# Performance work log

Hardware: AMD Instinct MI355X
Metric: run time of the kernel (lower is better)

Reference implementation:

```python
import jax, jax.numpy as jnp
import numpy as np

B, N, F_IN, F_OUT, H = 8, 1024, 256, 256, 4
HD = F_OUT // H  # head_dim = 64
NEG_SLOPE = 0.2


def setup_inputs() -> dict:
    key = jax.random.key(0)
    k1, k2, k3 = jax.random.split(key, 3)
    x = jax.random.normal(k1, (B, N, F_IN), dtype=jnp.float32)
    adj = jnp.ones((B, N, N), dtype=jnp.int32)
    # Linear weight, stored as [in, out] so h = x @ W
    W = jax.random.normal(k2, (F_IN, F_OUT), dtype=jnp.float32) / np.sqrt(F_IN)
    # attention vector a: [H, 2*head_dim], xavier-ish init
    a = jax.random.normal(k3, (H, 2 * HD), dtype=jnp.float32) * np.sqrt(2.0 / (H + 2 * HD))
    return {"x": x, "adj": adj, "W": W, "a": a}


def reference(x, adj, W, a):
    Bq, Nq, _ = x.shape
    h = (x @ W).reshape(Bq, Nq, H, HD).transpose(0, 2, 1, 3)  # [B,H,N,HD]
    a1, a2 = a[:, :HD], a[:, HD:]  # decompose concat: e_nm = h_n.a1 + h_m.a2
    s1 = jnp.einsum('bhnd,hd->bhn', h, a1)
    s2 = jnp.einsum('bhmd,hd->bhm', h, a2)
    e = jax.nn.leaky_relu(s1[:, :, :, None] + s2[:, :, None, :], NEG_SLOPE)  # [B,H,N,N]
    e = jnp.where(adj[:, None, :, :] == 0, -jnp.inf, e)
    attention = jax.nn.softmax(e, axis=-1)
    out = jnp.einsum('bhnm,bhmd->bhnd', attention, h)
    return out.transpose(0, 2, 1, 3).reshape(Bq, Nq, H * HD)
```

## Files before the change

### kernel.cpp

```cpp
#include <hip/hip_runtime.h>
#include <math.h>

#define H 4
#define HD 64
#define NN 1024
#define BB 8
#define FIN 256
#define FOUT 256

typedef _Float16 f16x8 __attribute__((ext_vector_type(8)));
typedef _Float16 f16x4 __attribute__((ext_vector_type(4)));
typedef _Float16 f16x2 __attribute__((ext_vector_type(2)));
typedef float f32x4 __attribute__((ext_vector_type(4)));

__device__ __forceinline__ unsigned fkey(float f) {
  unsigned u = __float_as_uint(f);
  return (u & 0x80000000u) ? ~u : (u | 0x80000000u);
}
__device__ __forceinline__ float fdecode(unsigned k) {
  unsigned u = (k & 0x80000000u) ? (k & 0x7fffffffu) : ~k;
  return __uint_as_float(u);
}

__global__ __launch_bounds__(256) void prep(const int* __restrict__ adj,
                                            unsigned* __restrict__ adjP,
                                            const float* __restrict__ W,
                                            _Float16* __restrict__ WT,
                                            unsigned* __restrict__ S2maxU) {
  __shared__ float tile[64][68];
  const int tid = threadIdx.x;
  if (blockIdx.x < 1024) {
    size_t widx = (size_t)blockIdx.x * 256 + tid;
    const int4* p = (const int4*)adj + widx * 8;
    int4 v[8];
#pragma unroll
    for (int i = 0; i < 8; ++i) v[i] = p[i];
    unsigned bits = 0;
#pragma unroll
    for (int i = 0; i < 8; ++i) {
      bits |= (v[i].x != 0 ? 1u : 0u) << (4 * i);
      bits |= (v[i].y != 0 ? 2u : 0u) << (4 * i);
      bits |= (v[i].z != 0 ? 4u : 0u) << (4 * i);
      bits |= (v[i].w != 0 ? 8u : 0u) << (4 * i);
    }
    adjP[widx] = bits;
  } else {
    if (blockIdx.x == 1024 && tid < 32) S2maxU[tid] = 0u;
    const int bx = blockIdx.x - 1024;
    const int k0 = (bx & 3) * 64, f0 = (bx >> 2) * 64;
    const int r = tid >> 4, c4 = (tid & 15) * 4;
#pragma unroll
    for (int p = 0; p < 4; ++p) {
      float4 v = *(const float4*)&W[(size_t)(k0 + p * 16 + r) * FOUT + f0 + c4];
      *(float4*)&tile[p * 16 + r][c4] = v;
    }
    __syncthreads();
    const int f = tid >> 2, kg = (tid & 3) * 16;
#pragma unroll
    for (int i = 0; i < 4; ++i) {
      f16x4 o;
#pragma unroll
      for (int j = 0; j < 4; ++j) o[j] = (_Float16)tile[kg + i * 4 + j][f];
      *(f16x4*)&WT[(size_t)(f0 + f) * FIN + k0 + kg + i * 4] = o;
    }
  }
}

__global__ __launch_bounds__(256) void gemm_xw(const float* __restrict__ x,
                                               const _Float16* __restrict__ WT,
                                               const float* __restrict__ a,
                                               _Float16* __restrict__ hT,
                                               float* __restrict__ s1_ws,
                                               float* __restrict__ s2_ws,
                                               unsigned* __restrict__ S2maxU) {
  __shared__ _Float16 wl[64][264];
  const int tid = threadIdx.x;
  const int lane = tid & 63, w = tid >> 6;
  const int c = lane & 15, q = lane >> 4;
  const int bn0 = blockIdx.x * 64;
  const int head = blockIdx.y;
  const int b = bn0 >> 10, nb = bn0 & 1023;
  const int bh = b * H + head;

  {
    const int row = tid >> 2, kseg = (tid & 3) * 64;
    const _Float16* wp = WT + (size_t)(head * 64 + row) * FIN + kseg;
#pragma unroll
    for (int i = 0; i < 8; ++i) {
      f16x8 t = *(const f16x8*)(wp + i * 8);
      *(f16x8*)&wl[row][kseg + i * 8] = t;
    }
  }
  __syncthreads();

  f32x4 acc[4];
#pragma unroll
  for (int t = 0; t < 4; ++t) acc[t] = (f32x4){0.f, 0.f, 0.f, 0.f};
  const float* xp = x + (size_t)(bn0 + w * 16 + c) * FIN + q * 8;
#pragma unroll
  for (int ks = 0; ks < 8; ++ks) {
    float4 xa = *(const float4*)(xp + ks * 32);
    float4 xb = *(const float4*)(xp + ks * 32 + 4);
    f16x8 af;
    af[0] = (_Float16)xa.x; af[1] = (_Float16)xa.y;
    af[2] = (_Float16)xa.z; af[3] = (_Float16)xa.w;
    af[4] = (_Float16)xb.x; af[5] = (_Float16)xb.y;
    af[6] = (_Float16)xb.z; af[7] = (_Float16)xb.w;
#pragma unroll
    for (int t = 0; t < 4; ++t) {
      f16x8 bf = *(const f16x8*)&wl[t * 16 + c][ks * 32 + q * 8];
      acc[t] = __builtin_amdgcn_mfma_f32_16x16x32_f16(af, bf, acc[t], 0, 0, 0);
    }
  }

  float a1v[4], a2v[4];
#pragma unroll
  for (int t = 0; t < 4; ++t) {
    a1v[t] = a[head * 2 * HD + t * 16 + c];
    a2v[t] = a[head * 2 * HD + HD + t * 16 + c];
  }
  float s1p[4] = {0.f, 0.f, 0.f, 0.f};
  float s2p[4] = {0.f, 0.f, 0.f, 0.f};
#pragma unroll
  for (int t = 0; t < 4; ++t) {
    f16x4 hv;
#pragma unroll
    for (int rr = 0; rr < 4; ++rr) {
      hv[rr] = (_Float16)acc[t][rr];
      s1p[rr] += acc[t][rr] * a1v[t];
      s2p[rr] += acc[t][rr] * a2v[t];
    }
    *(f16x4*)&hT[((size_t)(bh * 64 + t * 16 + c)) * NN + nb + w * 16 + q * 4] = hv;
  }
  float ms2 = -INFINITY;
#pragma unroll
  for (int rr = 0; rr < 4; ++rr) {
    float s1 = s1p[rr], s2 = s2p[rr];
#pragma unroll
    for (int off = 8; off; off >>= 1) {
      s1 += __shfl_xor(s1, off);
      s2 += __shfl_xor(s2, off);
    }
    ms2 = fmaxf(ms2, s2);
    if (c == 0) {
      int n = nb + w * 16 + q * 4 + rr;
      size_t idx = (size_t)bh * NN + n;
      s1_ws[idx] = s1;
      s2_ws[idx] = s2;
    }
  }
  ms2 = fmaxf(ms2, __shfl_xor(ms2, 16));
  ms2 = fmaxf(ms2, __shfl_xor(ms2, 32));
  if (lane == 0) atomicMax(&S2maxU[bh], fkey(ms2));
}

__global__ __launch_bounds__(256) void attn(const _Float16* __restrict__ hT,
                                            const float* __restrict__ s1_ws,
                                            const float* __restrict__ s2_ws,
                                            const unsigned* __restrict__ S2maxU,
                                            const unsigned* __restrict__ adjP,
                                            float* __restrict__ out) {
  __shared__ _Float16 u16[NN], v16[NN];
  __shared__ unsigned adjW[64][36];
  __shared__ int denseFlag;
  const int tid = threadIdx.x, lane = tid & 63, wv = tid >> 6;
  const int c = lane & 15, q = lane >> 4;
  const int ntile = blockIdx.x, bh = blockIdx.y;
  const int b = bh >> 2, head = bh & 3;
  const int n0 = ntile * 64;

  if (tid == 0) denseFlag = 1;
  __syncthreads();

  const float S2 = fdecode(S2maxU[bh]);
  {
    float4 s2a = *(const float4*)&s2_ws[(size_t)bh * NN + tid * 4];
    f16x4 ua, va;
    ua[0] = (_Float16)__expf(s2a.x - S2); va[0] = (_Float16)__expf(0.2f * (s2a.x - S2));
    ua[1] = (_Float16)__expf(s2a.y - S2); va[1] = (_Float16)__expf(0.2f * (s2a.y - S2));
    ua[2] = (_Float16)__expf(s2a.z - S2); va[2] = (_Float16)__expf(0.2f * (s2a.z - S2));
    ua[3] = (_Float16)__expf(s2a.w - S2); va[3] = (_Float16)__expf(0.2f * (s2a.w - S2));
    *(f16x4*)&u16[tid * 4] = ua;
    *(f16x4*)&v16[tid * 4] = va;
    const int row = tid >> 2, wo = (tid & 3) * 8;
    const uint4* ap = (const uint4*)(adjP + ((size_t)(b * NN + n0 + row)) * 32 + wo);
    uint4 m0 = ap[0], m1 = ap[1];
    *(uint4*)&adjW[row][wo] = m0;
    *(uint4*)&adjW[row][wo + 4] = m1;
    unsigned andall = m0.x & m0.y & m0.z & m0.w & m1.x & m1.y & m1.z & m1.w;
    if (andall != 0xffffffffu) atomicAnd(&denseFlag, 0);
  }
  __syncthreads();
  const int dense = denseFlag;

  f16x2 ar2[4], br2[4];
#pragma unroll
  for (int g = 0; g < 4; ++g) {
    float s1 = s1_ws[(size_t)bh * NN + n0 + g * 16 + c];
    float t = s1 + S2;
    float M = fmaxf(t, 0.2f * t);
    _Float16 A = (_Float16)__expf(t - M);
    _Float16 Bv = (_Float16)__expf(0.2f * t - M);
    ar2[g][0] = A; ar2[g][1] = A;
    br2[g][0] = Bv; br2[g][1] = Bv;
  }

  f32x4 acc[4], accL[4];
#pragma unroll
  for (int g = 0; g < 4; ++g) {
    acc[g] = (f32x4){0.f, 0.f, 0.f, 0.f};
    accL[g] = (f32x4){0.f, 0.f, 0.f, 0.f};
  }
  f16x8 bones;
  {
    _Float16 o = (c == 0) ? (_Float16)1.0f : (_Float16)0.0f;
#pragma unroll
    for (int j = 0; j < 8; ++j) bones[j] = o;
  }

  const _Float16* bp = hT + ((size_t)bh * 64 + wv * 16 + c) * NN + q * 8;
  f16x8 nbf = *(const f16x8*)bp;

  for (int kc4 = 0; kc4 < 8; ++kc4) {
    unsigned mrow[4][4];
    if (!dense) {
#pragma unroll
      for (int g = 0; g < 4; ++g) {
        uint4 t = *(const uint4*)&adjW[g * 16 + c][kc4 * 4];
        mrow[g][0] = t.x; mrow[g][1] = t.y; mrow[g][2] = t.z; mrow[g][3] = t.w;
      }
    }
#pragma unroll
    for (int kk = 0; kk < 4; ++kk) {
      const int kc = kc4 * 4 + kk;
      f16x8 bf = nbf;
      if (kc < 31) nbf = *(const f16x8*)(bp + (kc + 1) * 32);
      f16x8 u8 = *(const f16x8*)&u16[kc * 32 + q * 8];
      f16x8 v8 = *(const f16x8*)&v16[kc * 32 + q * 8];
      f16x2 up[4], vp[4];
#pragma unroll
      for (int j = 0; j < 4; ++j) {
        up[j][0] = u8[2 * j]; up[j][1] = u8[2 * j + 1];
        vp[j][0] = v8[2 * j]; vp[j][1] = v8[2 * j + 1];
      }
#pragma unroll
      for (int g = 0; g < 4; ++g) {
        f16x2 pp[4];
#pragma unroll
        for (int j = 0; j < 4; ++j)
          pp[j] = __builtin_elementwise_max(ar2[g] * up[j], br2[g] * vp[j]);
        if (!dense) {
          unsigned byte = (mrow[g][kk] >> (q * 8)) & 0xffu;
#pragma unroll
          for (int j = 0; j < 4; ++j) {
            unsigned pm = __builtin_bit_cast(unsigned, pp[j]);
            unsigned msk = (((byte >> (2 * j)) & 1u) ? 0x0000ffffu : 0u) |
                           (((byte >> (2 * j + 1)) & 1u) ? 0xffff0000u : 0u);
            pp[j] = __builtin_bit_cast(f16x2, pm & msk);
          }
        }
        union { f16x8 v8_; f16x2 v2_[4]; } au;
        au.v2_[0] = pp[0]; au.v2_[1] = pp[1]; au.v2_[2] = pp[2]; au.v2_[3] = pp[3];
        acc[g] = __builtin_amdgcn_mfma_f32_16x16x32_f16(au.v8_, bf, acc[g], 0, 0, 0);
        accL[g] = __builtin_amdgcn_mfma_f32_16x16x32_f16(au.v8_, bones, accL[g], 0, 0, 0);
      }
    }
  }

#pragma unroll
  for (int g = 0; g < 4; ++g) {
#pragma unroll
    for (int rr = 0; rr < 4; ++rr) {
      float Lrow = __shfl(accL[g][rr], q * 16);
      out[((size_t)(b * NN + n0 + g * 16 + q * 4 + rr)) * FOUT + head * 64 + wv * 16 + c] =
          acc[g][rr] / Lrow;
    }
  }
}

extern "C" void kernel_launch(void* const* d_in, const int* in_sizes, int n_in,
                              void* d_out, int out_size, void* d_ws, size_t ws_size,
                              hipStream_t stream) {
  const float* x = (const float*)d_in[0];
  const int* adj = (const int*)d_in[1];
  const float* W = (const float*)d_in[2];
  const float* a = (const float*)d_in[3];
  float* out = (float*)d_out;

  char* ws = (char*)d_ws;
  _Float16* hT = (_Float16*)ws;
  _Float16* WT = (_Float16*)(ws + (size_t)4 * 1024 * 1024);
  float* s1_ws = (float*)(ws + (size_t)4 * 1024 * 1024 + 128 * 1024);
  float* s2_ws = s1_ws + (size_t)BB * H * NN;
  unsigned* S2maxU = (unsigned*)(s2_ws + (size_t)BB * H * NN);
  unsigned* adjP = S2maxU + 64;

  prep<<<1040, 256, 0, stream>>>(adj, adjP, W, WT, S2maxU);
  gemm_xw<<<dim3(128, 4), 256, 0, stream>>>(x, WT, a, hT, s1_ws, s2_ws, S2maxU);
  attn<<<dim3(16, 32), 256, 0, stream>>>(hT, s1_ws, s2_ws, S2maxU, adjP, out);
}
```

Baseline: 120.3 us.

## Halve attn row tile to 32 to double grid size and occupancy

The attention kernel now processes 32 query rows per block instead of 64, launching twice as many blocks (1024 vs 512) so more of the GPU's compute units have work. It adds a launch-bounds occupancy hint, double-buffers the hT fragment loads two steps ahead, and replaces the final division with a reciprocal multiply. The cost is that each block recomputes the u/v exponentials and reloads the hT column tile for half as many rows, which doubles that redundant work and traffic.

```diff
diff --git a/kernel.cpp b/kernel.cpp
--- a/kernel.cpp
+++ b/kernel.cpp
@@ -154,20 +154,20 @@
   if (lane == 0) atomicMax(&S2maxU[bh], fkey(ms2));
 }
 
-__global__ __launch_bounds__(256) void attn(const _Float16* __restrict__ hT,
-                                            const float* __restrict__ s1_ws,
-                                            const float* __restrict__ s2_ws,
-                                            const unsigned* __restrict__ S2maxU,
-                                            const unsigned* __restrict__ adjP,
-                                            float* __restrict__ out) {
+__global__ __launch_bounds__(256, 4) void attn(const _Float16* __restrict__ hT,
+                                               const float* __restrict__ s1_ws,
+                                               const float* __restrict__ s2_ws,
+                                               const unsigned* __restrict__ S2maxU,
+                                               const unsigned* __restrict__ adjP,
+                                               float* __restrict__ out) {
   __shared__ _Float16 u16[NN], v16[NN];
-  __shared__ unsigned adjW[64][36];
+  __shared__ unsigned adjW[32][36];
   __shared__ int denseFlag;
   const int tid = threadIdx.x, lane = tid & 63, wv = tid >> 6;
   const int c = lane & 15, q = lane >> 4;
   const int ntile = blockIdx.x, bh = blockIdx.y;
   const int b = bh >> 2, head = bh & 3;
-  const int n0 = ntile * 64;
+  const int n0 = ntile * 32;
 
   if (tid == 0) denseFlag = 1;
   __syncthreads();
@@ -182,20 +182,17 @@
     ua[3] = (_Float16)__expf(s2a.w - S2); va[3] = (_Float16)__expf(0.2f * (s2a.w - S2));
     *(f16x4*)&u16[tid * 4] = ua;
     *(f16x4*)&v16[tid * 4] = va;
-    const int row = tid >> 2, wo = (tid & 3) * 8;
-    const uint4* ap = (const uint4*)(adjP + ((size_t)(b * NN + n0 + row)) * 32 + wo);
-    uint4 m0 = ap[0], m1 = ap[1];
+    const int row = tid >> 3, wo = (tid & 7) * 4;
+    uint4 m0 = *(const uint4*)(adjP + ((size_t)(b * NN + n0 + row)) * 32 + wo);
     *(uint4*)&adjW[row][wo] = m0;
-    *(uint4*)&adjW[row][wo + 4] = m1;
-    unsigned andall = m0.x & m0.y & m0.z & m0.w & m1.x & m1.y & m1.z & m1.w;
-    if (andall != 0xffffffffu) atomicAnd(&denseFlag, 0);
+    if ((m0.x & m0.y & m0.z & m0.w) != 0xffffffffu) atomicAnd(&denseFlag, 0);
   }
   __syncthreads();
   const int dense = denseFlag;
 
-  f16x2 ar2[4], br2[4];
-#pragma unroll
-  for (int g = 0; g < 4; ++g) {
+  f16x2 ar2[2], br2[2];
+#pragma unroll
+  for (int g = 0; g < 2; ++g) {
     float s1 = s1_ws[(size_t)bh * NN + n0 + g * 16 + c];
     float t = s1 + S2;
     float M = fmaxf(t, 0.2f * t);
@@ -205,9 +202,9 @@
     br2[g][0] = Bv; br2[g][1] = Bv;
   }
 
-  f32x4 acc[4], accL[4];
-#pragma unroll
-  for (int g = 0; g < 4; ++g) {
+  f32x4 acc[2], accL[2];
+#pragma unroll
+  for (int g = 0; g < 2; ++g) {
     acc[g] = (f32x4){0.f, 0.f, 0.f, 0.f};
     accL[g] = (f32x4){0.f, 0.f, 0.f, 0.f};
   }
@@ -219,61 +216,57 @@
   }
 
   const _Float16* bp = hT + ((size_t)bh * 64 + wv * 16 + c) * NN + q * 8;
-  f16x8 nbf = *(const f16x8*)bp;
-
-  for (int kc4 = 0; kc4 < 8; ++kc4) {
-    unsigned mrow[4][4];
+  f16x8 nbf[2];
+  nbf[0] = *(const f16x8*)bp;
+  nbf[1] = *(const f16x8*)(bp + 32);
+
+  for (int kc = 0; kc < 32; ++kc) {
+    f16x8 bf = nbf[kc & 1];
+    if (kc < 30) nbf[kc & 1] = *(const f16x8*)(bp + (kc + 2) * 32);
+    f16x8 u8 = *(const f16x8*)&u16[kc * 32 + q * 8];
+    f16x8 v8 = *(const f16x8*)&v16[kc * 32 + q * 8];
+    f16x2 up[4], vp[4];
+#pragma unroll
+    for (int j = 0; j < 4; ++j) {
+      up[j][0] = u8[2 * j]; up[j][1] = u8[2 * j + 1];
+      vp[j][0] = v8[2 * j]; vp[j][1] = v8[2 * j + 1];
+    }
+    unsigned mword[2];
     if (!dense) {
 #pragma unroll
-      for (int g = 0; g < 4; ++g) {
-        uint4 t = *(const uint4*)&adjW[g * 16 + c][kc4 * 4];
-        mrow[g][0] = t.x; mrow[g][1] = t.y; mrow[g][2] = t.z; mrow[g][3] = t.w;
+      for (int g = 0; g < 2; ++g) mword[g] = adjW[g * 16 + c][kc];
+    }
+#pragma unroll
+    for (int g = 0; g < 2; ++g) {
+      f16x2 pp[4];
+#pragma unroll
+      for (int j = 0; j < 4; ++j)
+        pp[j] = __builtin_elementwise_max(ar2[g] * up[j], br2[g] * vp[j]);
+      if (!dense) {
+        unsigned byte = (mword[g] >> (q * 8)) & 0xffu;
+#pragma unroll
+        for (int j = 0; j < 4; ++j) {
+          unsigned pm = __builtin_bit_cast(unsigned, pp[j]);
+          unsigned msk = (((byte >> (2 * j)) & 1u) ? 0x0000ffffu : 0u) |
+                         (((byte >> (2 * j + 1)) & 1u) ? 0xffff0000u : 0u);
+          pp[j] = __builtin_bit_cast(f16x2, pm & msk);
+        }
       }
-    }
-#pragma unroll
-    for (int kk = 0; kk < 4; ++kk) {
-      const int kc = kc4 * 4 + kk;
-      f16x8 bf = nbf;
-      if (kc < 31) nbf = *(const f16x8*)(bp + (kc + 1) * 32);
-      f16x8 u8 = *(const f16x8*)&u16[kc * 32 + q * 8];
-      f16x8 v8 = *(const f16x8*)&v16[kc * 32 + q * 8];
-      f16x2 up[4], vp[4];
-#pragma unroll
-      for (int j = 0; j < 4; ++j) {
-        up[j][0] = u8[2 * j]; up[j][1] = u8[2 * j + 1];
-        vp[j][0] = v8[2 * j]; vp[j][1] = v8[2 * j + 1];
-      }
-#pragma unroll
-      for (int g = 0; g < 4; ++g) {
-        f16x2 pp[4];
-#pragma unroll
-        for (int j = 0; j < 4; ++j)
-          pp[j] = __builtin_elementwise_max(ar2[g] * up[j], br2[g] * vp[j]);
-        if (!dense) {
-          unsigned byte = (mrow[g][kk] >> (q * 8)) & 0xffu;
-#pragma unroll
-          for (int j = 0; j < 4; ++j) {
-            unsigned pm = __builtin_bit_cast(unsigned, pp[j]);
-            unsigned msk = (((byte >> (2 * j)) & 1u) ? 0x0000ffffu : 0u) |
-                           (((byte >> (2 * j + 1)) & 1u) ? 0xffff0000u : 0u);
-            pp[j] = __builtin_bit_cast(f16x2, pm & msk);
-          }
-        }
-        union { f16x8 v8_; f16x2 v2_[4]; } au;
-        au.v2_[0] = pp[0]; au.v2_[1] = pp[1]; au.v2_[2] = pp[2]; au.v2_[3] = pp[3];
-        acc[g] = __builtin_amdgcn_mfma_f32_16x16x32_f16(au.v8_, bf, acc[g], 0, 0, 0);
-        accL[g] = __builtin_amdgcn_mfma_f32_16x16x32_f16(au.v8_, bones, accL[g], 0, 0, 0);
-      }
-    }
-  }
-
-#pragma unroll
-  for (int g = 0; g < 4; ++g) {
+      union { f16x8 v8_; f16x2 v2_[4]; } au;
+      au.v2_[0] = pp[0]; au.v2_[1] = pp[1]; au.v2_[2] = pp[2]; au.v2_[3] = pp[3];
+      acc[g] = __builtin_amdgcn_mfma_f32_16x16x32_f16(au.v8_, bf, acc[g], 0, 0, 0);
+      accL[g] = __builtin_amdgcn_mfma_f32_16x16x32_f16(au.v8_, bones, accL[g], 0, 0, 0);
+    }
+  }
+
+#pragma unroll
+  for (int g = 0; g < 2; ++g) {
 #pragma unroll
     for (int rr = 0; rr < 4; ++rr) {
       float Lrow = __shfl(accL[g][rr], q * 16);
+      float il = __builtin_amdgcn_rcpf(Lrow);
       out[((size_t)(b * NN + n0 + g * 16 + q * 4 + rr)) * FOUT + head * 64 + wv * 16 + c] =
-          acc[g][rr] / Lrow;
+          acc[g][rr] * il;
     }
   }
 }
@@ -297,5 +290,5 @@
 
   prep<<<1040, 256, 0, stream>>>(adj, adjP, W, WT, S2maxU);
   gemm_xw<<<dim3(128, 4), 256, 0, stream>>>(x, WT, a, hT, s1_ws, s2_ws, S2maxU);
-  attn<<<dim3(16, 32), 256, 0, stream>>>(hT, s1_ws, s2_ws, S2maxU, adjP, out);
-}
+  attn<<<dim3(32, 32), 256, 0, stream>>>(hT, s1_ws, s2_ws, S2maxU, adjP, out);
+}
```

After: 353.3 us. 194% more time.
